# Performance work log

Measured on AMD Instinct MI355X. Metric: run time of the kernel, lower is better.

## Reference

```python
import jax, jax.numpy as jnp
import numpy as np

T, B, E, H = 2048, 2, 1024, 16
HD = E // H
NEG = -1e9  # large negative for causal additive mask


def setup_inputs() -> dict:
    key = jax.random.key(0)
    ks = jax.random.split(key, 6)
    s = 0.02
    query = jax.random.normal(ks[0], (T, B, E), jnp.float32)
    # causal additive mask, as commonly passed to this module's attn_mask arg
    attn_mask = jnp.triu(jnp.full((T, T), NEG, jnp.float32), k=1)
    key_padding_mask = jnp.zeros((B, T), jnp.bool_)
    Wq = jax.random.normal(ks[1], (E, E), jnp.float32) * s
    Wk = jax.random.normal(ks[2], (E, E), jnp.float32) * s
    Wv = jax.random.normal(ks[3], (E, E), jnp.float32) * s
    Wo = jax.random.normal(ks[4], (E, E), jnp.float32) * s
    bq = jnp.zeros((E,), jnp.float32)
    bk = jnp.zeros((E,), jnp.float32)
    bv = jnp.zeros((E,), jnp.float32)
    bo = jnp.zeros((E,), jnp.float32)
    return {"query": query, "attn_mask": attn_mask, "key_padding_mask": key_padding_mask,
            "Wq": Wq, "bq": bq, "Wk": Wk, "bk": bk, "Wv": Wv, "bv": bv, "Wo": Wo, "bo": bo}


def _shape(x):
    # [T, B, E] -> [B*H, T, HD]; E splits as (H, HD), flat index = b*H + h
    return x.reshape(T, B * H, HD).transpose(1, 0, 2)


def reference(query, attn_mask, key_padding_mask, Wq, bq, Wk, bk, Wv, bv, Wo, bo):
    scaling = HD ** -0.5
    q = (query @ Wq.T + bq) * scaling  # scale q as in torch code
    k = query @ Wk.T + bk              # self-attention path (static_kv=False)
    v = query @ Wv.T + bv
    q, k, v = _shape(q), _shape(k), _shape(v)            # [B*H, T, HD]
    w = jnp.einsum('bth,bsh->bts', q, k)                  # [B*H, T, S]
    w = w.reshape(B, H, T, T) + attn_mask                 # additive mask broadcast
    w = jnp.where(key_padding_mask[:, None, None, :], -jnp.inf, w)
    p = jax.nn.softmax(w, axis=-1).reshape(B * H, T, T)   # dropout p=0 (eval)
    o = jnp.einsum('bts,bsh->bth', p, v)                  # [B*H, T, HD]
    o = o.transpose(1, 0, 2).reshape(T, B, E)
    return o @ Wo.T + bo
```

## Files before the change

### kernel.cpp

```cpp
#include <hip/hip_runtime.h>

#define Tt 2048
#define Bb 2
#define Ee 1024
#define Hh 16
#define HD 64
#define BH 32

typedef __attribute__((ext_vector_type(8))) short short8;
typedef __attribute__((ext_vector_type(4))) short short4v;
typedef __attribute__((ext_vector_type(8))) __bf16 bf16x8;
typedef __attribute__((ext_vector_type(4))) float floatx4;

#define OFF_X  0
#define OFF_WQ 4194304
#define OFF_WK 5242880
#define OFF_WV 6291456
#define OFF_WO 7340032
#define OFF_Q  8388608
#define OFF_K  12582912
#define OFF_V  16777216
#define OFF_O  20971520

__device__ __forceinline__ short f2bf(float f) {
  union { float f; unsigned u; } a; a.f = f;
  unsigned r = a.u + 0x7fffu + ((a.u >> 16) & 1u);
  return (short)(r >> 16);
}

__device__ __forceinline__ floatx4 mfma16(short8 a, short8 b, floatx4 c) {
  return __builtin_amdgcn_mfma_f32_16x16x32_bf16(
      __builtin_bit_cast(bf16x8, a), __builtin_bit_cast(bf16x8, b), c, 0, 0, 0);
}

__device__ __forceinline__ void gl_lds16(const short* g, short* l) {
  __builtin_amdgcn_global_load_lds(
      (const __attribute__((address_space(1))) void*)g,
      (__attribute__((address_space(3))) void*)l, 16, 0, 0);
}

__device__ __forceinline__ uint2 exppack(floatx4 s, float& l) {
  float p0 = __builtin_amdgcn_exp2f(s[0]);
  float p1 = __builtin_amdgcn_exp2f(s[1]);
  float p2 = __builtin_amdgcn_exp2f(s[2]);
  float p3 = __builtin_amdgcn_exp2f(s[3]);
  l += (p0 + p1) + (p2 + p3);
  unsigned u0 = __builtin_bit_cast(unsigned, p0) + 0x8000u;
  unsigned u1 = __builtin_bit_cast(unsigned, p1) + 0x8000u;
  unsigned u2 = __builtin_bit_cast(unsigned, p2) + 0x8000u;
  unsigned u3 = __builtin_bit_cast(unsigned, p3) + 0x8000u;
  uint2 pk;
  pk.x = __builtin_amdgcn_perm(u1, u0, 0x07060302u);
  pk.y = __builtin_amdgcn_perm(u3, u2, 0x07060302u);
  return pk;
}

__global__ __launch_bounds__(256)
void convert_kernel(const float* __restrict__ x, const float* __restrict__ wq,
                    const float* __restrict__ wk, const float* __restrict__ wv,
                    const float* __restrict__ wo, short* __restrict__ dst)
{
  const int i4 = blockIdx.x * 256 + threadIdx.x;
  const int f = i4 * 4;
  const float* src;
  int local;
  if (f < 4194304) { src = x; local = f; }
  else {
    int gg = f - 4194304;
    int wsel = gg >> 20;
    local = gg & 1048575;
    src = (wsel == 0) ? wq : (wsel == 1) ? wk : (wsel == 2) ? wv : wo;
  }
  floatx4 v = *reinterpret_cast<const floatx4*>(src + local);
  short4 o;
  o.x = f2bf(v[0]); o.y = f2bf(v[1]); o.z = f2bf(v[2]); o.w = f2bf(v[3]);
  *reinterpret_cast<short4*>(dst + f) = o;
}

__global__ __launch_bounds__(256, 2)
void qkv_kernel(short* __restrict__ ws, const float* __restrict__ bq,
                const float* __restrict__ bk, const float* __restrict__ bv)
{
  __shared__ short smem[2][8192];
  const int t = threadIdx.x;
  const int lane = t & 63;
  const int w = t >> 6;
  const int g = lane >> 4, c = lane & 15;
  const int rb = blockIdx.x * 128;
  const int cb = blockIdx.y * 128;
  const int rw = (w >> 1) * 64, cw2 = (w & 1) * 64;

  const short* gA[2]; const short* gB[2]; int oC[2];
#pragma unroll
  for (int i = 0; i < 2; i++) {
    const int cid = t + 256 * i;
    const int row = cid >> 2;
    const int lch = (cid & 3) ^ ((row + (row >> 2)) & 3);
    gA[i] = ws + OFF_X + (rb + row) * 1024 + lch * 8;
    gB[i] = ws + OFF_WQ + (cb + row) * 1024 + lch * 8;
    oC[i] = cid * 8;
  }
  const int xr = (g ^ ((c + (c >> 2)) & 3)) * 8;

  floatx4 acc[4][4];
#pragma unroll
  for (int i = 0; i < 4; i++)
#pragma unroll
    for (int j = 0; j < 4; j++) acc[i][j] = (floatx4){0.f, 0.f, 0.f, 0.f};

#pragma unroll
  for (int i = 0; i < 2; i++) {
    gl_lds16(gA[i], &smem[0][oC[i]]);
    gl_lds16(gB[i], &smem[0][4096 + oC[i]]);
  }
  __syncthreads();

  for (int kt = 0; kt < 32; kt++) {
    const int cur = kt & 1;
    if (kt < 31) {
      const int kn = (kt + 1) * 32;
#pragma unroll
      for (int i = 0; i < 2; i++) {
        gl_lds16(gA[i] + kn, &smem[cur ^ 1][oC[i]]);
        gl_lds16(gB[i] + kn, &smem[cur ^ 1][4096 + oC[i]]);
      }
    }
    short8 af[4], bf[4];
#pragma unroll
    for (int mi = 0; mi < 4; mi++)
      af[mi] = *reinterpret_cast<const short8*>(&smem[cur][(rw + mi * 16 + c) * 32 + xr]);
#pragma unroll
    for (int ni = 0; ni < 4; ni++)
      bf[ni] = *reinterpret_cast<const short8*>(&smem[cur][4096 + (cw2 + ni * 16 + c) * 32 + xr]);
#pragma unroll
    for (int mi = 0; mi < 4; mi++)
#pragma unroll
      for (int ni = 0; ni < 4; ni++)
        acc[mi][ni] = mfma16(af[mi], bf[ni], acc[mi][ni]);
    __syncthreads();
  }

  const int m = cb >> 10;
  const int lcb = cb & 1023;
  if (m < 2) {
#pragma unroll
    for (int ni = 0; ni < 4; ni++) {
      const int lc = lcb + cw2 + ni * 16 + c;
      const int h = lc >> 6, d = lc & 63;
      const float bcol = (m == 0 ? bq : bk)[lc];
      const int dpart = (d >> 3) * 128 + (d & 7);
#pragma unroll
      for (int mi = 0; mi < 4; mi++)
#pragma unroll
        for (int r = 0; r < 4; r++) {
          const int row = rb + rw + mi * 16 + g * 4 + r;
          const int tt = row >> 1, b = row & 1;
          float v = acc[mi][ni][r] + bcol;
          if (m == 0) v *= 0.18033688f;
          ws[(m == 0 ? OFF_Q : OFF_K) + (b * Hh + h) * 131072
             + (tt >> 4) * 1024 + dpart + (tt & 15) * 8] = f2bf(v);
        }
    }
  } else {
    short* vt = &smem[0][0];
    const int hb = lcb >> 6;
    for (int b = 0; b < 2; b++) {
      __syncthreads();
#pragma unroll
      for (int ni = 0; ni < 4; ni++) {
        const int lcol = cw2 + ni * 16 + c;
        const float bcol = bv[lcb + lcol];
#pragma unroll
        for (int mi = 0; mi < 4; mi++)
#pragma unroll
          for (int rr = 0; rr < 2; rr++) {
            const int r = rr * 2 + b;
            const int rloc = rw + mi * 16 + g * 4 + r;
            vt[lcol * 72 + (rloc >> 1)] = f2bf(acc[mi][ni][r] + bcol);
          }
      }
      __syncthreads();
#pragma unroll
      for (int i = 0; i < 4; i++) {
        const int u = t + 256 * i;
        const int lcol = u >> 3, seg = u & 7;
        short8 vv = *reinterpret_cast<const short8*>(vt + lcol * 72 + seg * 8);
        const int h = hb + (lcol >> 6), d = lcol & 63;
        *reinterpret_cast<short8*>(ws + OFF_V + ((b * Hh + h)) * 131072
                                   + ((rb >> 5) + (seg >> 1)) * 1024
                                   + d * 16 + (seg & 1) * 8) = vv;
      }
    }
  }
}

__global__ __launch_bounds__(256, 2)
void gemm_o(const short* __restrict__ ws, const float* __restrict__ bo,
            float* __restrict__ dout)
{
  __shared__ short smem[2][8192];
  const int t = threadIdx.x;
  const int lane = t & 63;
  const int w = t >> 6;
  const int g = lane >> 4, c = lane & 15;
  const int rb = blockIdx.x * 128;
  const int cb = blockIdx.y * 128;
  const int rw = (w >> 1) * 64, cw2 = (w & 1) * 64;

  const short* gA[2]; const short* gB[2]; int oC[2];
#pragma unroll
  for (int i = 0; i < 2; i++) {
    const int cid = t + 256 * i;
    const int row = cid >> 2;
    const int lch = (cid & 3) ^ ((row + (row >> 2)) & 3);
    gA[i] = ws + OFF_O + (rb + row) * 1024 + lch * 8;
    gB[i] = ws + OFF_WO + (cb + row) * 1024 + lch * 8;
    oC[i] = cid * 8;
  }
  const int xr = (g ^ ((c + (c >> 2)) & 3)) * 8;

  floatx4 acc[4][4];
#pragma unroll
  for (int i = 0; i < 4; i++)
#pragma unroll
    for (int j = 0; j < 4; j++) acc[i][j] = (floatx4){0.f, 0.f, 0.f, 0.f};

#pragma unroll
  for (int i = 0; i < 2; i++) {
    gl_lds16(gA[i], &smem[0][oC[i]]);
    gl_lds16(gB[i], &smem[0][4096 + oC[i]]);
  }
  __syncthreads();

  for (int kt = 0; kt < 32; kt++) {
    const int cur = kt & 1;
    if (kt < 31) {
      const int kn = (kt + 1) * 32;
#pragma unroll
      for (int i = 0; i < 2; i++) {
        gl_lds16(gA[i] + kn, &smem[cur ^ 1][oC[i]]);
        gl_lds16(gB[i] + kn, &smem[cur ^ 1][4096 + oC[i]]);
      }
    }
    short8 af[4], bf[4];
#pragma unroll
    for (int mi = 0; mi < 4; mi++)
      af[mi] = *reinterpret_cast<const short8*>(&smem[cur][(rw + mi * 16 + c) * 32 + xr]);
#pragma unroll
    for (int ni = 0; ni < 4; ni++)
      bf[ni] = *reinterpret_cast<const short8*>(&smem[cur][4096 + (cw2 + ni * 16 + c) * 32 + xr]);
#pragma unroll
    for (int mi = 0; mi < 4; mi++)
#pragma unroll
      for (int ni = 0; ni < 4; ni++)
        acc[mi][ni] = mfma16(af[mi], bf[ni], acc[mi][ni]);
    __syncthreads();
  }

#pragma unroll
  for (int ni = 0; ni < 4; ni++) {
    const int col = cb + cw2 + ni * 16 + c;
    const float bcol = bo[col];
#pragma unroll
    for (int mi = 0; mi < 4; mi++)
#pragma unroll
      for (int r = 0; r < 4; r++) {
        const int row = rb + rw + mi * 16 + g * 4 + r;
        dout[row * 1024 + col] = acc[mi][ni][r] + bcol;
      }
  }
}

__global__ __launch_bounds__(256, 2)
void attn_kernel(short* __restrict__ ws, const unsigned char* __restrict__ kpm)
{
  __shared__ __align__(16) short smem[32768];

  const int t = threadIdx.x;
  const int lane = t & 63;
  const int w = t >> 6;
  const int g = lane >> 4, c = lane & 15;
  const int bh = blockIdx.x;
  const int b = bh >> 4;
  const int h = bh & 15;
  const int qt = 31 - (int)blockIdx.y;
  const int qrow0 = qt * 64;

  const short* Qp = ws + OFF_Q + bh * 131072;
  const short* Kp = ws + OFF_K + bh * 131072;
  const short* Vp = ws + OFF_V + bh * 131072;

  short8 qf[4][2];
  const short* Qc = Qp + (qrow0 >> 4) * 1024 + lane * 8;
#pragma unroll
  for (int qs = 0; qs < 4; qs++) {
    qf[qs][0] = *reinterpret_cast<const short8*>(Qc + qs * 1024);
    qf[qs][1] = *reinterpret_cast<const short8*>(Qc + qs * 1024 + 512);
  }

  const uint4* kpv = reinterpret_cast<const uint4*>(kpm + b * Tt);
  uint4 k0v = kpv[lane * 2], k1v = kpv[lane * 2 + 1];
  const bool nz = (k0v.x | k0v.y | k0v.z | k0v.w | k1v.x | k1v.y | k1v.z | k1v.w) != 0;
  const unsigned long long kpany = __ballot(nz);

  float lt[4] = {0.f, 0.f, 0.f, 0.f};
  floatx4 acc[4][4];
#pragma unroll
  for (int i = 0; i < 4; i++)
#pragma unroll
    for (int j = 0; j < 4; j++) acc[i][j] = (floatx4){0.f, 0.f, 0.f, 0.f};

  const short* Ksrc = Kp + w * 1024 + lane * 8;
  const short* Vsrc = Vp + w * 1024 + lane * 8;
  const int woff = w * 1024;

  const int NT = qt + 1;
  const int NP = (NT + 1) >> 1;

  {
    const int tb0 = (NT > 1) ? 1 : 0;
    gl_lds16(Ksrc,                  &smem[woff]);
    gl_lds16(Ksrc + 512,            &smem[woff + 512]);
    gl_lds16(Ksrc + tb0 * 4096,       &smem[4096 + woff]);
    gl_lds16(Ksrc + tb0 * 4096 + 512, &smem[4096 + woff + 512]);
    gl_lds16(Vsrc,                  &smem[8192 + woff]);
    gl_lds16(Vsrc + 512,            &smem[8192 + woff + 512]);
    gl_lds16(Vsrc + tb0 * 4096,       &smem[12288 + woff]);
    gl_lds16(Vsrc + tb0 * 4096 + 512, &smem[12288 + woff + 512]);
  }

  for (int pp = 0; pp < NP; pp++) {
    const int so = (pp & 1) * 16384 + woff;
    if (pp + 1 < NP) {
      const int na = 2 * pp + 2;
      const int nb = (na + 1 < NT) ? na + 1 : na;
      const int no = ((pp + 1) & 1) * 16384 + woff;
      gl_lds16(Ksrc + na * 4096,       &smem[no]);
      gl_lds16(Ksrc + na * 4096 + 512, &smem[no + 512]);
      gl_lds16(Ksrc + nb * 4096,       &smem[no + 4096]);
      gl_lds16(Ksrc + nb * 4096 + 512, &smem[no + 4096 + 512]);
      gl_lds16(Vsrc + na * 4096,       &smem[no + 8192]);
      gl_lds16(Vsrc + na * 4096 + 512, &smem[no + 8192 + 512]);
      gl_lds16(Vsrc + nb * 4096,       &smem[no + 12288]);
      gl_lds16(Vsrc + nb * 4096 + 512, &smem[no + 12288 + 512]);
      asm volatile("s_waitcnt vmcnt(8)" ::: "memory");
    } else {
      asm volatile("s_waitcnt vmcnt(0)" ::: "memory");
    }
    __builtin_amdgcn_sched_barrier(0);

    const int ta = 2 * pp, tb = 2 * pp + 1;

    const short* kfa = &smem[so + g * 128 + c * 8];
    short8 ka0 = *reinterpret_cast<const short8*>(kfa);
    short8 ka1 = *reinterpret_cast<const short8*>(kfa + 512);
    __builtin_amdgcn_s_setprio(1);
    floatx4 sa[4];
#pragma unroll
    for (int qs = 0; qs < 4; qs++) {
      floatx4 z = (floatx4){0.f, 0.f, 0.f, 0.f};
      z = mfma16(ka0, qf[qs][0], z);
      z = mfma16(ka1, qf[qs][1], z);
      sa[qs] = z;
    }
    __builtin_amdgcn_s_setprio(0);
    if ((kpany >> (2 * ta)) & 3ULL) {
#pragma unroll
      for (int r = 0; r < 4; r++)
        if (kpm[b * Tt + ta * 64 + w * 16 + g * 4 + r] != 0) {
#pragma unroll
          for (int qs = 0; qs < 4; qs++) sa[qs][r] = -1e30f;
        }
    }
    if (ta == qt) {
      const int kl = w * 16 + g * 4;
#pragma unroll
      for (int qs = 0; qs < 4; qs++)
#pragma unroll
        for (int r = 0; r < 4; r++)
          if (kl + r > qs * 16 + c) sa[qs][r] = -1e30f;
    }
    uint2 ua[4];
#pragma unroll
    for (int qs = 0; qs < 4; qs++) ua[qs] = exppack(sa[qs], lt[qs]);

    uint2 ub[4];
    ub[0] = ub[1] = ub[2] = ub[3] = (uint2){0u, 0u};
    if (tb < NT) {
      const short* kfb = &smem[so + 4096 + g * 128 + c * 8];
      short8 kb0 = *reinterpret_cast<const short8*>(kfb);
      short8 kb1 = *reinterpret_cast<const short8*>(kfb + 512);
      __builtin_amdgcn_s_setprio(1);
      floatx4 sb[4];
#pragma unroll
      for (int qs = 0; qs < 4; qs++) {
        floatx4 z = (floatx4){0.f, 0.f, 0.f, 0.f};
        z = mfma16(kb0, qf[qs][0], z);
        z = mfma16(kb1, qf[qs][1], z);
        sb[qs] = z;
      }
      __builtin_amdgcn_s_setprio(0);
      if ((kpany >> (2 * tb)) & 3ULL) {
#pragma unroll
        for (int r = 0; r < 4; r++)
          if (kpm[b * Tt + tb * 64 + w * 16 + g * 4 + r] != 0) {
#pragma unroll
            for (int qs = 0; qs < 4; qs++) sb[qs][r] = -1e30f;
          }
      }
      if (tb == qt) {
        const int kl = w * 16 + g * 4;
#pragma unroll
        for (int qs = 0; qs < 4; qs++)
#pragma unroll
          for (int r = 0; r < 4; r++)
            if (kl + r > qs * 16 + c) sb[qs][r] = -1e30f;
      }
#pragma unroll
      for (int qs = 0; qs < 4; qs++) ub[qs] = exppack(sb[qs], lt[qs]);
    }

    short8 pa8[4];
#pragma unroll
    for (int qs = 0; qs < 4; qs++) {
      uint4 uu; uu.x = ua[qs].x; uu.y = ua[qs].y; uu.z = ub[qs].x; uu.w = ub[qs].y;
      pa8[qs] = __builtin_bit_cast(short8, uu);
    }
    const short* vfa = &smem[so + 8192 + c * 16 + g * 4];
    const short* vfb = &smem[so + 12288 + c * 16 + g * 4];
    __builtin_amdgcn_s_setprio(1);
#pragma unroll
    for (int dt = 0; dt < 4; dt++) {
      short4v va_ = *reinterpret_cast<const short4v*>(vfa + dt * 256);
      short4v vb_ = *reinterpret_cast<const short4v*>(vfb + dt * 256);
      short8 vv;
      vv[0] = va_[0]; vv[1] = va_[1]; vv[2] = va_[2]; vv[3] = va_[3];
      vv[4] = vb_[0]; vv[5] = vb_[1]; vv[6] = vb_[2]; vv[7] = vb_[3];
#pragma unroll
      for (int qs = 0; qs < 4; qs++)
        acc[qs][dt] = mfma16(pa8[qs], vv, acc[qs][dt]);
    }
    __builtin_amdgcn_s_setprio(0);
  }

#pragma unroll
  for (int qs = 0; qs < 4; qs++) {
    lt[qs] += __shfl_xor(lt[qs], 16);
    lt[qs] += __shfl_xor(lt[qs], 32);
  }

  __syncthreads();
  float* bufA = reinterpret_cast<float*>(smem);
  float* bufB = bufA + 4352;
  float* Ls   = bufA + 8704;
  if (g == 0) {
#pragma unroll
    for (int qs = 0; qs < 4; qs++) Ls[w * 64 + qs * 16 + c] = lt[qs];
  }
  float* mybuf = (w < 2) ? bufA : bufB;
  if ((w & 1) == 0) {
#pragma unroll
    for (int qs = 0; qs < 4; qs++)
#pragma unroll
      for (int dt = 0; dt < 4; dt++)
#pragma unroll
        for (int r = 0; r < 4; r++)
          mybuf[(qs * 16 + g * 4 + r) * 68 + dt * 16 + c] = acc[qs][dt][r];
  }
  __syncthreads();
  if (w & 1) {
#pragma unroll
    for (int qs = 0; qs < 4; qs++)
#pragma unroll
      for (int dt = 0; dt < 4; dt++)
#pragma unroll
        for (int r = 0; r < 4; r++)
          mybuf[(qs * 16 + g * 4 + r) * 68 + dt * 16 + c] += acc[qs][dt][r];
  }
  __syncthreads();

  const int row = w * 16 + (lane >> 2);
  const int dseg = (lane & 3) * 16;
  const float inv = 1.f / (Ls[row] + Ls[64 + row] + Ls[128 + row] + Ls[192 + row]);
  short* op = ws + OFF_O + ((qrow0 + row) * Bb + b) * Ee + h * 64 + dseg;
#pragma unroll
  for (int i = 0; i < 2; i++) {
    floatx4 a0 = *reinterpret_cast<const floatx4*>(&bufA[row * 68 + dseg + i * 8]);
    floatx4 a1 = *reinterpret_cast<const floatx4*>(&bufA[row * 68 + dseg + i * 8 + 4]);
    floatx4 b0 = *reinterpret_cast<const floatx4*>(&bufB[row * 68 + dseg + i * 8]);
    floatx4 b1 = *reinterpret_cast<const floatx4*>(&bufB[row * 68 + dseg + i * 8 + 4]);
    short8 s;
#pragma unroll
    for (int j = 0; j < 4; j++) s[j] = f2bf((a0[j] + b0[j]) * inv);
#pragma unroll
    for (int j = 0; j < 4; j++) s[4 + j] = f2bf((a1[j] + b1[j]) * inv);
    *reinterpret_cast<short8*>(op + i * 8) = s;
  }
}

extern "C" void kernel_launch(void* const* d_in, const int* in_sizes, int n_in,
                              void* d_out, int out_size, void* d_ws, size_t ws_size,
                              hipStream_t stream)
{
  const float* query = (const float*)d_in[0];
  const unsigned char* kpm = (const unsigned char*)d_in[2];
  const float* Wq = (const float*)d_in[3];
  const float* bq = (const float*)d_in[4];
  const float* Wk = (const float*)d_in[5];
  const float* bk = (const float*)d_in[6];
  const float* Wv = (const float*)d_in[7];
  const float* bv = (const float*)d_in[8];
  const float* Wo = (const float*)d_in[9];
  const float* bo = (const float*)d_in[10];
  short* ws = (short*)d_ws;
  float* out = (float*)d_out;

  convert_kernel<<<dim3(8192), dim3(256), 0, stream>>>(query, Wq, Wk, Wv, Wo, ws);
  qkv_kernel<<<dim3(32, 24), dim3(256), 0, stream>>>(ws, bq, bk, bv);
  attn_kernel<<<dim3(32, 32), dim3(256), 0, stream>>>(ws, kpm);
  gemm_o<<<dim3(32, 8), dim3(256), 0, stream>>>(ws, bo, out);
}
```

Before: 184.6 us.

## Stage Q/K projection output through LDS and use triple-buffered K/V tile ring

The Q/K projection epilogue now writes each half-tile into shared memory and then emits coalesced 16-byte stores into the blocked head layout, replacing scattered 2-byte global writes. The attention kernel replaces the two-stage double buffer of tile pairs with a three-slot ring of single 64-key tiles. Prefetches are issued one tile at a time with finer vmcnt waits, and V fragments are loaded into registers early, so a slot can be refilled while the next tile is consumed. This shrinks attention LDS from 64KB to 48KB, which could raise occupancy. The cost is more waitcnt points and more complex buffer bookkeeping.

```diff
diff --git a/kernel.cpp b/kernel.cpp
--- a/kernel.cpp
+++ b/kernel.cpp
@@ -143,23 +143,36 @@
   const int m = cb >> 10;
   const int lcb = cb & 1023;
   if (m < 2) {
-#pragma unroll
-    for (int ni = 0; ni < 4; ni++) {
-      const int lc = lcb + cw2 + ni * 16 + c;
-      const int h = lc >> 6, d = lc & 63;
-      const float bcol = (m == 0 ? bq : bk)[lc];
-      const int dpart = (d >> 3) * 128 + (d & 7);
-#pragma unroll
-      for (int mi = 0; mi < 4; mi++)
-#pragma unroll
-        for (int r = 0; r < 4; r++) {
-          const int row = rb + rw + mi * 16 + g * 4 + r;
-          const int tt = row >> 1, b = row & 1;
-          float v = acc[mi][ni][r] + bcol;
-          if (m == 0) v *= 0.18033688f;
-          ws[(m == 0 ? OFF_Q : OFF_K) + (b * Hh + h) * 131072
-             + (tt >> 4) * 1024 + dpart + (tt & 15) * 8] = f2bf(v);
+    short* vt = &smem[0][0];
+    const float sc = (m == 0) ? 0.18033688f : 1.0f;
+    const int baseo = (m == 0) ? OFF_Q : OFF_K;
+    for (int hb = 0; hb < 2; hb++) {
+      __syncthreads();
+      if ((w >> 1) == hb) {
+#pragma unroll
+        for (int ni = 0; ni < 4; ni++) {
+          const int lc = cw2 + ni * 16 + c;
+          const float bcol = (m == 0 ? bq : bk)[lcb + lc];
+#pragma unroll
+          for (int mi = 0; mi < 4; mi++)
+#pragma unroll
+            for (int r = 0; r < 4; r++)
+              vt[(mi * 16 + g * 4 + r) * 136 + lc] = f2bf((acc[mi][ni][r] + bcol) * sc);
         }
+      }
+      __syncthreads();
+#pragma unroll
+      for (int i = 0; i < 4; i++) {
+        const int u = t + 256 * i;
+        const int ttl = u & 31, bsel = (u >> 5) & 1, lc8 = u >> 6;
+        const int rl = ttl * 2 + bsel;
+        const int row = rb + hb * 64 + rl;
+        const int tt = row >> 1, bb = row & 1;
+        const int hh = (lcb + lc8 * 8) >> 6;
+        short8 vv = *reinterpret_cast<const short8*>(vt + rl * 136 + lc8 * 8);
+        *reinterpret_cast<short8*>(ws + baseo + (bb * Hh + hh) * 131072
+            + (tt >> 4) * 1024 + (lc8 & 7) * 128 + (tt & 15) * 8) = vv;
+      }
     }
   } else {
     short* vt = &smem[0][0];
@@ -274,7 +287,7 @@
 __global__ __launch_bounds__(256, 2)
 void attn_kernel(short* __restrict__ ws, const unsigned char* __restrict__ kpm)
 {
-  __shared__ __align__(16) short smem[32768];
+  __shared__ __align__(16) short smem[24576];
 
   const int t = threadIdx.x;
   const int lane = t & 63;
@@ -317,41 +330,39 @@
   const int NT = qt + 1;
   const int NP = (NT + 1) >> 1;
 
-  {
-    const int tb0 = (NT > 1) ? 1 : 0;
-    gl_lds16(Ksrc,                  &smem[woff]);
-    gl_lds16(Ksrc + 512,            &smem[woff + 512]);
-    gl_lds16(Ksrc + tb0 * 4096,       &smem[4096 + woff]);
-    gl_lds16(Ksrc + tb0 * 4096 + 512, &smem[4096 + woff + 512]);
-    gl_lds16(Vsrc,                  &smem[8192 + woff]);
-    gl_lds16(Vsrc + 512,            &smem[8192 + woff + 512]);
-    gl_lds16(Vsrc + tb0 * 4096,       &smem[12288 + woff]);
-    gl_lds16(Vsrc + tb0 * 4096 + 512, &smem[12288 + woff + 512]);
-  }
-
+  gl_lds16(Ksrc,       &smem[woff]);
+  gl_lds16(Ksrc + 512, &smem[woff + 512]);
+  gl_lds16(Vsrc,       &smem[4096 + woff]);
+  gl_lds16(Vsrc + 512, &smem[4096 + woff + 512]);
+  if (NT > 1) {
+    gl_lds16(Ksrc + 4096,       &smem[8192 + woff]);
+    gl_lds16(Ksrc + 4096 + 512, &smem[8192 + woff + 512]);
+    gl_lds16(Vsrc + 4096,       &smem[8192 + 4096 + woff]);
+    gl_lds16(Vsrc + 4096 + 512, &smem[8192 + 4096 + 512 + woff]);
+  }
+
+  int co = 0;
   for (int pp = 0; pp < NP; pp++) {
-    const int so = (pp & 1) * 16384 + woff;
-    if (pp + 1 < NP) {
-      const int na = 2 * pp + 2;
-      const int nb = (na + 1 < NT) ? na + 1 : na;
-      const int no = ((pp + 1) & 1) * 16384 + woff;
-      gl_lds16(Ksrc + na * 4096,       &smem[no]);
-      gl_lds16(Ksrc + na * 4096 + 512, &smem[no + 512]);
-      gl_lds16(Ksrc + nb * 4096,       &smem[no + 4096]);
-      gl_lds16(Ksrc + nb * 4096 + 512, &smem[no + 4096 + 512]);
-      gl_lds16(Vsrc + na * 4096,       &smem[no + 8192]);
-      gl_lds16(Vsrc + na * 4096 + 512, &smem[no + 8192 + 512]);
-      gl_lds16(Vsrc + nb * 4096,       &smem[no + 12288]);
-      gl_lds16(Vsrc + nb * 4096 + 512, &smem[no + 12288 + 512]);
+    const int ta = 2 * pp, tb = ta + 1;
+    int cbuf = co + 8192;  if (cbuf >= 24576) cbuf -= 24576;
+    int cn   = co + 16384; if (cn   >= 24576) cn   -= 24576;
+
+    if (ta + 2 < NT) {
+      const short* ks = Ksrc + (ta + 2) * 4096;
+      const short* vs = Vsrc + (ta + 2) * 4096;
+      gl_lds16(ks,       &smem[cn + woff]);
+      gl_lds16(ks + 512, &smem[cn + woff + 512]);
+      gl_lds16(vs,       &smem[cn + 4096 + woff]);
+      gl_lds16(vs + 512, &smem[cn + 4096 + woff + 512]);
       asm volatile("s_waitcnt vmcnt(8)" ::: "memory");
+    } else if (tb < NT) {
+      asm volatile("s_waitcnt vmcnt(4)" ::: "memory");
     } else {
       asm volatile("s_waitcnt vmcnt(0)" ::: "memory");
     }
     __builtin_amdgcn_sched_barrier(0);
 
-    const int ta = 2 * pp, tb = 2 * pp + 1;
-
-    const short* kfa = &smem[so + g * 128 + c * 8];
+    const short* kfa = &smem[co + woff + g * 128 + c * 8];
     short8 ka0 = *reinterpret_cast<const short8*>(kfa);
     short8 ka1 = *reinterpret_cast<const short8*>(kfa + 512);
     __builtin_amdgcn_s_setprio(1);
@@ -383,11 +394,34 @@
     uint2 ua[4];
 #pragma unroll
     for (int qs = 0; qs < 4; qs++) ua[qs] = exppack(sa[qs], lt[qs]);
+    const short* vfa = &smem[co + 4096 + woff + c * 16 + g * 4];
+    short4v vA[4];
+#pragma unroll
+    for (int dt = 0; dt < 4; dt++)
+      vA[dt] = *reinterpret_cast<const short4v*>(vfa + dt * 256);
 
     uint2 ub[4];
     ub[0] = ub[1] = ub[2] = ub[3] = (uint2){0u, 0u};
+    short4v vB[4];
+#pragma unroll
+    for (int dt = 0; dt < 4; dt++) vB[dt] = vA[dt];
     if (tb < NT) {
-      const short* kfb = &smem[so + 4096 + g * 128 + c * 8];
+      if (tb + 2 < NT) {
+        const short* ks = Ksrc + (tb + 2) * 4096;
+        const short* vs = Vsrc + (tb + 2) * 4096;
+        gl_lds16(ks,       &smem[co + woff]);
+        gl_lds16(ks + 512, &smem[co + woff + 512]);
+        gl_lds16(vs,       &smem[co + 4096 + woff]);
+        gl_lds16(vs + 512, &smem[co + 4096 + woff + 512]);
+        asm volatile("s_waitcnt vmcnt(8)" ::: "memory");
+      } else if (tb + 1 < NT) {
+        asm volatile("s_waitcnt vmcnt(4)" ::: "memory");
+      } else {
+        asm volatile("s_waitcnt vmcnt(0)" ::: "memory");
+      }
+      __builtin_amdgcn_sched_barrier(0);
+
+      const short* kfb = &smem[cbuf + woff + g * 128 + c * 8];
       short8 kb0 = *reinterpret_cast<const short8*>(kfb);
       short8 kb1 = *reinterpret_cast<const short8*>(kfb + 512);
       __builtin_amdgcn_s_setprio(1);
@@ -418,6 +452,10 @@
       }
 #pragma unroll
       for (int qs = 0; qs < 4; qs++) ub[qs] = exppack(sb[qs], lt[qs]);
+      const short* vfb = &smem[cbuf + 4096 + woff + c * 16 + g * 4];
+#pragma unroll
+      for (int dt = 0; dt < 4; dt++)
+        vB[dt] = *reinterpret_cast<const short4v*>(vfb + dt * 256);
     }
 
     short8 pa8[4];
@@ -426,21 +464,19 @@
       uint4 uu; uu.x = ua[qs].x; uu.y = ua[qs].y; uu.z = ub[qs].x; uu.w = ub[qs].y;
       pa8[qs] = __builtin_bit_cast(short8, uu);
     }
-    const short* vfa = &smem[so + 8192 + c * 16 + g * 4];
-    const short* vfb = &smem[so + 12288 + c * 16 + g * 4];
     __builtin_amdgcn_s_setprio(1);
 #pragma unroll
     for (int dt = 0; dt < 4; dt++) {
-      short4v va_ = *reinterpret_cast<const short4v*>(vfa + dt * 256);
-      short4v vb_ = *reinterpret_cast<const short4v*>(vfb + dt * 256);
       short8 vv;
-      vv[0] = va_[0]; vv[1] = va_[1]; vv[2] = va_[2]; vv[3] = va_[3];
-      vv[4] = vb_[0]; vv[5] = vb_[1]; vv[6] = vb_[2]; vv[7] = vb_[3];
+      vv[0] = vA[dt][0]; vv[1] = vA[dt][1]; vv[2] = vA[dt][2]; vv[3] = vA[dt][3];
+      vv[4] = vB[dt][0]; vv[5] = vB[dt][1]; vv[6] = vB[dt][2]; vv[7] = vB[dt][3];
 #pragma unroll
       for (int qs = 0; qs < 4; qs++)
         acc[qs][dt] = mfma16(pa8[qs], vv, acc[qs][dt]);
     }
     __builtin_amdgcn_s_setprio(0);
+
+    co = cn;
   }
 
 #pragma unroll
```

New measurement: 184.1 us. About the same (-0.3%).
